# Kernel optimization log

Measured on AMD Instinct MI355X. Metric: run time of the kernel, lower is better.

Reference implementation:

```python
import jax, jax.numpy as jnp
import numpy as np

NFEAT = 128
NHID = 64
NLAYER = 3
N_NODES = 50000
N_EDGES = 800000
N_GRAPHS = 512
BN_EPS = 1e-5


def _bn(x, gamma, beta):
    # BatchNorm1d in training mode: biased batch stats over the node axis.
    m = x.mean(axis=0)
    v = x.var(axis=0)
    return (x - m) * jax.lax.rsqrt(v + BN_EPS) * gamma + beta


def _pool(x, batch):
    # global_mean_pool: segment mean over graph ids.
    s = jax.ops.segment_sum(x, batch, num_segments=N_GRAPHS)
    c = jax.ops.segment_sum(jnp.ones((x.shape[0], 1), x.dtype), batch, num_segments=N_GRAPHS)
    return s / jnp.maximum(c, 1.0)


def setup_inputs() -> dict:
    key = jax.random.key(0)
    ks = jax.random.split(key, 16)
    x = jax.random.normal(ks[0], (N_NODES, NFEAT), dtype=jnp.float32)
    edge_index = jax.random.randint(ks[1], (2, N_EDGES), 0, N_NODES, dtype=jnp.int64)
    batch = jnp.sort(jax.random.randint(ks[2], (N_NODES,), 0, N_GRAPHS, dtype=jnp.int64))
    s_in = 1.0 / np.sqrt(NFEAT)
    s_h = 1.0 / np.sqrt(NHID)
    return {
        "x": x,
        "edge_index": edge_index,
        "batch": batch,
        "Wt": jax.random.uniform(ks[3], (NFEAT, NHID), jnp.float32, -s_in, s_in),
        "bt": jax.random.uniform(ks[4], (NHID,), jnp.float32, -s_in, s_in),
        "gt": jnp.ones((NHID,), jnp.float32),
        "bet": jnp.zeros((NHID,), jnp.float32),
        "W1": jax.random.uniform(ks[5], (NLAYER, NHID, NHID), jnp.float32, -s_h, s_h),
        "b1": jax.random.uniform(ks[6], (NLAYER, NHID), jnp.float32, -s_h, s_h),
        "W2": jax.random.uniform(ks[7], (NLAYER, NHID, NHID), jnp.float32, -s_h, s_h),
        "b2": jax.random.uniform(ks[8], (NLAYER, NHID), jnp.float32, -s_h, s_h),
        "g": jnp.ones((NLAYER, NHID), jnp.float32),
        "be": jnp.zeros((NLAYER, NHID), jnp.float32),
    }


def reference(x, edge_index, batch, Wt, bt, gt, bet, W1, b1, W2, b2, g, be):
    n = x.shape[0]
    src, dst = edge_index[0], edge_index[1]
    # input transform: Linear + BN
    h = _bn(x @ Wt + bt, gt, bet)
    embeds = [_pool(h, batch)]
    for l in range(NLAYER):
        # GINConv, eps=0: mlp(x_i + sum_{j->i} x_j); flow source->target
        agg = jax.ops.segment_sum(h[src], dst, num_segments=n)
        z = h + agg
        z = jax.nn.relu(z @ W1[l] + b1[l]) @ W2[l] + b2[l]
        h = jax.nn.relu(_bn(z, g[l], be[l]))
        embeds.append(_pool(h, batch))
    return jnp.stack(embeds)  # [NLAYER+1, N_GRAPHS, NHID]
```

## Files before the change

### kernel.cpp

```cpp
#include <hip/hip_runtime.h>

#define NFEAT   128
#define NHID    64
#define NLAYER  3
#define NNODES  50000
#define NEDGES  800000
#define NGRAPHS 512
#define BN_EPS  1e-5f
#define MLPB    1563
#define CAP     64
#define PADW    68
#define FILLB   2048
#define SETUPB  83

typedef unsigned short u16;
typedef __attribute__((ext_vector_type(8))) short bf8;
typedef __attribute__((ext_vector_type(4))) float f32x4;

__device__ inline float b2f(u16 v) { return __uint_as_float(((unsigned)v) << 16); }
__device__ inline u16 f2b(float f) {
    unsigned u = __float_as_uint(f);
    return (u16)((u + 0x7FFF + ((u >> 16) & 1)) >> 16);
}
__device__ inline bf8 ldb8(const u16* p) {
    union { uint2 a[2]; bf8 v; } u;
    u.a[0] = *(const uint2*)p;
    u.a[1] = *(const uint2*)(p + 4);
    return u.v;
}
__device__ inline bf8 ldb8g(const u16* p) {
    union { uint4 a; bf8 v; } u;
    u.a = *(const uint4*)p;
    return u.v;
}
__device__ inline void add4(float* a, const uint2 v) {
    a[0] += __uint_as_float(v.x << 16);
    a[1] += __uint_as_float(v.x & 0xFFFF0000u);
    a[2] += __uint_as_float(v.y << 16);
    a[3] += __uint_as_float(v.y & 0xFFFF0000u);
}
__device__ inline void unp4(float* a, const uint2 v) {
    a[0] = __uint_as_float(v.x << 16);
    a[1] = __uint_as_float(v.x & 0xFFFF0000u);
    a[2] = __uint_as_float(v.y << 16);
    a[3] = __uint_as_float(v.y & 0xFFFF0000u);
}
__device__ inline void unp8(float* a, const uint4 v) {
    a[0] = __uint_as_float(v.x << 16);
    a[1] = __uint_as_float(v.x & 0xFFFF0000u);
    a[2] = __uint_as_float(v.y << 16);
    a[3] = __uint_as_float(v.y & 0xFFFF0000u);
    a[4] = __uint_as_float(v.z << 16);
    a[5] = __uint_as_float(v.z & 0xFFFF0000u);
    a[6] = __uint_as_float(v.w << 16);
    a[7] = __uint_as_float(v.w & 0xFFFF0000u);
}
__device__ inline uint2 pack4(float a, float b, float c, float d) {
    uint2 r;
    r.x = (unsigned)f2b(a) | ((unsigned)f2b(b) << 16);
    r.y = (unsigned)f2b(c) | ((unsigned)f2b(d) << 16);
    return r;
}

__global__ __launch_bounds__(256) void k_build(const int* __restrict__ ei,
                                               int* __restrict__ deg,
                                               u16* __restrict__ col,
                                               const float* __restrict__ Wt,
                                               const float* __restrict__ W1,
                                               const float* __restrict__ W2,
                                               const int* __restrict__ batch,
                                               u16* __restrict__ wtin,
                                               u16* __restrict__ wt,
                                               int* __restrict__ gstart) {
    int tid = threadIdx.x;
    if (blockIdx.x < FILLB) {
        int rangeId = blockIdx.x & 7, chunk = blockIdx.x >> 3;
        int lo = rangeId * (NNODES / 8), hi = lo + (NNODES / 8);
        int ebeg = chunk * (NEDGES / 256), eend = ebeg + (NEDGES / 256);
        int e = ebeg + tid;
        for (; e + 7 * 256 < eend; e += 8 * 256) {
            int d[8];
#pragma unroll
            for (int i = 0; i < 8; ++i) d[i] = ei[NEDGES + e + i * 256];
#pragma unroll
            for (int i = 0; i < 8; ++i) {
                if (d[i] >= lo && d[i] < hi) {
                    int s = atomicAdd(&deg[d[i]], 1);
                    if (s < CAP) col[d[i] * CAP + s] = (u16)ei[e + i * 256];
                }
            }
        }
        for (; e < eend; e += 256) {
            int dst = ei[NEDGES + e];
            if (dst >= lo && dst < hi) {
                int s = atomicAdd(&deg[dst], 1);
                if (s < CAP) col[dst * CAP + s] = (u16)ei[e];
            }
        }
        return;
    }
    int idx = (blockIdx.x - FILLB) * 256 + tid;
    if (idx < NFEAT * NHID) {
        int n = idx >> 7, k = idx & 127;
        wtin[n * NFEAT + k] = f2b(Wt[k * NHID + n]);
        return;
    }
    idx -= NFEAT * NHID;
    if (idx < NLAYER * NHID * NHID) {
        int l = idx >> 12, rem = idx & 4095, n = rem >> 6, k = rem & 63;
        wt[l * 8192 + n * 64 + k]        = f2b(W1[l * 4096 + k * 64 + n]);
        wt[l * 8192 + 4096 + n * 64 + k] = f2b(W2[l * 4096 + k * 64 + n]);
        return;
    }
    idx -= NLAYER * NHID * NHID;
    if (idx <= NGRAPHS) {
        if (idx == NGRAPHS) { gstart[NGRAPHS] = NNODES; return; }
        int lo = 0, hi = NNODES;
        while (lo < hi) {
            int mid = (lo + hi) >> 1;
            if (batch[mid] < idx) lo = mid + 1; else hi = mid;
        }
        gstart[idx] = lo;
    }
}

__global__ __launch_bounds__(256) void k_gemm_in(const float* __restrict__ x,
                                                 const u16* __restrict__ wtin,
                                                 const float* __restrict__ bt,
                                                 u16* __restrict__ zout,
                                                 float* __restrict__ partials) {
    __shared__ u16 sx[32][132];
    __shared__ float ps[128];
    int tid = threadIdx.x;
    int base = blockIdx.x * 32;
#pragma unroll
    for (int i = 0; i < 4; ++i) {
        int idx = i * 256 + tid;
        int row = idx >> 5, kq = idx & 31;
        int rc = min(base + row, NNODES - 1);
        float4 v = ((const float4*)(x + (long long)rc * NFEAT))[kq];
        *(uint2*)&sx[row][kq * 4] = pack4(v.x, v.y, v.z, v.w);
    }
    __syncthreads();
    int w = tid >> 6, lane = tid & 63;
    int m = lane & 15, g = lane >> 4;
    int ncol = w * 16 + m;
    bool hiv = (base + 16 < NNODES);
    float bb = bt[ncol];
    f32x4 cl = {bb, bb, bb, bb}, ch = {bb, bb, bb, bb};
    const u16* wn = wtin + ncol * NFEAT;
#pragma unroll
    for (int s = 0; s < 4; ++s) {
        int k0 = s * 32 + g * 8;
        bf8 B  = ldb8g(wn + k0);
        bf8 Al = ldb8(&sx[m][k0]);
        bf8 Ah = ldb8(&sx[16 + m][k0]);
        cl = __builtin_amdgcn_mfma_f32_16x16x32_bf16(Al, B, cl, 0, 0, 0);
        ch = __builtin_amdgcn_mfma_f32_16x16x32_bf16(Ah, B, ch, 0, 0, 0);
    }
    float s1 = cl[0] + cl[1] + cl[2] + cl[3];
    float s2 = cl[0] * cl[0] + cl[1] * cl[1] + cl[2] * cl[2] + cl[3] * cl[3];
    if (hiv) {
        s1 += ch[0] + ch[1] + ch[2] + ch[3];
        s2 += ch[0] * ch[0] + ch[1] * ch[1] + ch[2] * ch[2] + ch[3] * ch[3];
    }
    s1 += __shfl_xor(s1, 16, 64); s1 += __shfl_xor(s1, 32, 64);
    s2 += __shfl_xor(s2, 16, 64); s2 += __shfl_xor(s2, 32, 64);
    if (lane < 16) {
        ps[w * 16 + lane] = s1;
        ps[64 + w * 16 + lane] = s2;
    }
#pragma unroll
    for (int i = 0; i < 4; ++i) {
        zout[(base + g * 4 + i) * NHID + ncol] = f2b(cl[i]);
        if (hiv) zout[(base + 16 + g * 4 + i) * NHID + ncol] = f2b(ch[i]);
    }
    __syncthreads();
    if (tid < 128) partials[blockIdx.x * 128 + tid] = ps[tid];
}

__global__ __launch_bounds__(256) void k_red(const float* __restrict__ partials,
                                             float* __restrict__ stats, int np) {
    __shared__ float red[4];
    int c = blockIdx.x, t = threadIdx.x;
    float s = 0.f;
    for (int i = t; i < np; i += 256) s += partials[i * 128 + c];
#pragma unroll
    for (int off = 32; off >= 1; off >>= 1) s += __shfl_xor(s, off, 64);
    if ((t & 63) == 0) red[t >> 6] = s;
    __syncthreads();
    if (t == 0) stats[c] = red[0] + red[1] + red[2] + red[3];
}

__global__ __launch_bounds__(256) void k_bnh(const u16* __restrict__ z,
                                             const float* __restrict__ stats,
                                             const float* __restrict__ gamma,
                                             const float* __restrict__ beta,
                                             u16* __restrict__ h) {
    int idx = blockIdx.x * 256 + threadIdx.x;
    if (idx >= NNODES * NHID / 8) return;
    int j0 = (idx & 7) * 8;
    uint4 v = ((const uint4*)z)[idx];
    float o[8];
    unp8(o, v);
#pragma unroll
    for (int k = 0; k < 8; ++k) {
        int j = j0 + k;
        float m = stats[j] * (1.0f / NNODES);
        float var = stats[64 + j] * (1.0f / NNODES) - m * m;
        float sc = rsqrtf(var + BN_EPS) * gamma[j];
        o[k] = fmaxf(fmaf(o[k], sc, beta[j] - m * sc), 0.f);
    }
    uint4 w;
    uint2 p0 = pack4(o[0], o[1], o[2], o[3]);
    uint2 p1 = pack4(o[4], o[5], o[6], o[7]);
    w.x = p0.x; w.y = p0.y; w.z = p1.x; w.w = p1.y;
    ((uint4*)h)[idx] = w;
}

__global__ __launch_bounds__(256) void k_poolfin(const u16* __restrict__ z,
                                                 const float* __restrict__ stats,
                                                 const float* __restrict__ gamma,
                                                 const float* __restrict__ beta,
                                                 const int* __restrict__ gstart,
                                                 const float* __restrict__ poolacc,
                                                 float* __restrict__ out) {
    if (blockIdx.x >= NGRAPHS) {
        int idx = (int)(blockIdx.x - NGRAPHS) * 256 + threadIdx.x;
        if (idx < NLAYER * NGRAPHS * NHID) {
            int g = (idx >> 6) & (NGRAPHS - 1);
            float cnt = (float)(gstart[g + 1] - gstart[g]);
            out[idx] = poolacc[idx] / fmaxf(cnt, 1.0f);
        }
        return;
    }
    __shared__ float4 red[4][16];
    int gph = blockIdx.x;
    int lane = threadIdx.x & 63, w = threadIdx.x >> 6;
    int c = lane & 15, ws = lane >> 4;
    int slot = w * 4 + ws;
    int j0 = c * 4;
    float sc[4], sh[4];
#pragma unroll
    for (int k = 0; k < 4; ++k) {
        int j = j0 + k;
        float m = stats[j] * (1.0f / NNODES);
        float var = stats[64 + j] * (1.0f / NNODES) - m * m;
        sc[k] = rsqrtf(var + BN_EPS) * gamma[j];
        sh[k] = beta[j] - m * sc[k];
    }
    const ushort4* z4 = (const ushort4*)z;
    int s0 = gstart[gph], e0 = gstart[gph + 1];
    float a[4] = {0.f, 0.f, 0.f, 0.f};
    for (int r = s0 + slot; r < e0; r += 16) {
        ushort4 v = z4[r * 16 + c];
        a[0] += fmaxf(fmaf(b2f(v.x), sc[0], sh[0]), 0.f);
        a[1] += fmaxf(fmaf(b2f(v.y), sc[1], sh[1]), 0.f);
        a[2] += fmaxf(fmaf(b2f(v.z), sc[2], sh[2]), 0.f);
        a[3] += fmaxf(fmaf(b2f(v.w), sc[3], sh[3]), 0.f);
    }
#pragma unroll
    for (int k = 0; k < 4; ++k) {
        a[k] += __shfl_xor(a[k], 16, 64);
        a[k] += __shfl_xor(a[k], 32, 64);
    }
    if (lane < 16) red[w][c] = make_float4(a[0], a[1], a[2], a[3]);
    __syncthreads();
    if (threadIdx.x < 16) {
        float4 r0 = red[0][threadIdx.x], r1 = red[1][threadIdx.x];
        float4 r2 = red[2][threadIdx.x], r3 = red[3][threadIdx.x];
        float inv = 1.0f / fmaxf((float)(e0 - s0), 1.0f);
        float* o = &out[NLAYER * NGRAPHS * NHID + gph * NHID + threadIdx.x * 4];
        o[0] = (r0.x + r1.x + r2.x + r3.x) * inv;
        o[1] = (r0.y + r1.y + r2.y + r3.y) * inv;
        o[2] = (r0.z + r1.z + r2.z + r3.z) * inv;
        o[3] = (r0.w + r1.w + r2.w + r3.w) * inv;
    }
}

template <int AFFINE>
__global__ __launch_bounds__(512) void k_mlp(const u16* __restrict__ hin,
                                             const float* __restrict__ stats,
                                             const float* __restrict__ gamma,
                                             const float* __restrict__ beta,
                                             const int* __restrict__ batch,
                                             const int* __restrict__ deg,
                                             const u16* __restrict__ col,
                                             const u16* __restrict__ w1t,
                                             const float* __restrict__ b1,
                                             const u16* __restrict__ w2t,
                                             const float* __restrict__ b2,
                                             u16* __restrict__ zout,
                                             float* __restrict__ partials,
                                             float* __restrict__ poolacc) {
    __shared__ u16 szb[32][PADW];
    __shared__ u16 stb[32][PADW];
    __shared__ float ps2[2][128];
    int tid = threadIdx.x;
    int w = tid >> 6, lane = tid & 63;
    int nq = lane >> 4, c = lane & 15;
    int node = w * 4 + nq;
    int base = blockIdx.x * 32;
    int r = base + node;
    bool rv = (r < NNODES);
    int rc = rv ? r : (NNODES - 1);
    const uint2* h8 = (const uint2*)hin;

    float sc[4], sh[4];
    if (AFFINE) {
#pragma unroll
        for (int k = 0; k < 4; ++k) {
            int j = c * 4 + k;
            float m = stats[j] * (1.0f / NNODES);
            float var = stats[64 + j] * (1.0f / NNODES) - m * m;
            sc[k] = rsqrtf(var + BN_EPS) * gamma[j];
            sh[k] = beta[j] - m * sc[k];
        }
    }

    float acc[4], acc2[4] = {0, 0, 0, 0};
    float selfh[4];
    {
        uint2 sv = h8[rc * 16 + c];
        unp4(acc, sv);
#pragma unroll
        for (int k = 0; k < 4; ++k)
            selfh[k] = AFFINE ? fmaf(acc[k], sc[k], sh[k]) : acc[k];
    }
    int dd = rv ? min(deg[r], CAP) : 0;
    {
        const u16* cp = col + rc * CAP;
        int t = 0;
        for (; t + 8 <= dd; t += 8) {
            uint4 iv = *(const uint4*)(cp + t);
            int s0 = iv.x & 0xFFFF, s1 = iv.x >> 16;
            int s2 = iv.y & 0xFFFF, s3 = iv.y >> 16;
            int s4 = iv.z & 0xFFFF, s5 = iv.z >> 16;
            int s6 = iv.w & 0xFFFF, s7 = iv.w >> 16;
            uint2 v0 = h8[s0 * 16 + c];
            uint2 v1 = h8[s1 * 16 + c];
            uint2 v2 = h8[s2 * 16 + c];
            uint2 v3 = h8[s3 * 16 + c];
            uint2 v4 = h8[s4 * 16 + c];
            uint2 v5 = h8[s5 * 16 + c];
            uint2 v6 = h8[s6 * 16 + c];
            uint2 v7 = h8[s7 * 16 + c];
            add4(acc, v0); add4(acc2, v1); add4(acc, v2); add4(acc2, v3);
            add4(acc, v4); add4(acc2, v5); add4(acc, v6); add4(acc2, v7);
        }
        if (t + 4 <= dd) {
            uint2 iv = *(const uint2*)(cp + t);
            int s0 = iv.x & 0xFFFF, s1 = iv.x >> 16;
            int s2 = iv.y & 0xFFFF, s3 = iv.y >> 16;
            uint2 v0 = h8[s0 * 16 + c];
            uint2 v1 = h8[s1 * 16 + c];
            uint2 v2 = h8[s2 * 16 + c];
            uint2 v3 = h8[s3 * 16 + c];
            add4(acc, v0); add4(acc2, v1); add4(acc, v2); add4(acc2, v3);
            t += 4;
        }
        for (; t < dd; ++t) {
            uint2 v0 = h8[(int)cp[t] * 16 + c];
            add4(acc, v0);
        }
    }
    {
        float zv[4];
#pragma unroll
        for (int k = 0; k < 4; ++k) {
            float s = acc[k] + acc2[k];
            zv[k] = AFFINE ? fmaf(s, sc[k], (float)(1 + dd) * sh[k]) : s;
            if (!rv) zv[k] = 0.f;
        }
        *(uint2*)&szb[node][c * 4] = pack4(zv[0], zv[1], zv[2], zv[3]);
    }

    int m = lane & 15, g = lane >> 4;
    int half = w >> 2, cg = w & 3;
    int ncol = cg * 16 + m;
    const u16* w1n = w1t + ncol * 64;
    const u16* w2n = w2t + ncol * 64;
    bf8 B0 = ldb8g(w1n + g * 8);
    bf8 B1 = ldb8g(w1n + 32 + g * 8);
    bf8 D0 = ldb8g(w2n + g * 8);
    bf8 D1 = ldb8g(w2n + 32 + g * 8);

    {
        int r0 = base + w * 4;
        int myg = rv ? batch[r] : -1;
        int g_lo = batch[min(r0, NNODES - 1)];
        int g_hi = batch[min(r0 + 3, NNODES - 1)];
        for (int gg = g_lo; gg <= g_hi; ++gg) {
            float v[4];
#pragma unroll
            for (int k = 0; k < 4; ++k) {
                v[k] = (myg == gg) ? selfh[k] : 0.f;
                v[k] += __shfl_xor(v[k], 16, 64);
                v[k] += __shfl_xor(v[k], 32, 64);
            }
            if (lane < 16) {
                float* p = &poolacc[gg * NHID + lane * 4];
#pragma unroll
                for (int k = 0; k < 4; ++k) atomicAdd(p + k, v[k]);
            }
        }
    }
    __syncthreads();

    bool hiv = (base + 16 < NNODES);
    bool halfv = (half == 0) || hiv;
    bf8 A0 = ldb8(&szb[half * 16 + m][g * 8]);
    bf8 A1 = ldb8(&szb[half * 16 + m][32 + g * 8]);
    float bb1 = b1[ncol];
    f32x4 c1 = {bb1, bb1, bb1, bb1};
    c1 = __builtin_amdgcn_mfma_f32_16x16x32_bf16(A0, B0, c1, 0, 0, 0);
    c1 = __builtin_amdgcn_mfma_f32_16x16x32_bf16(A1, B1, c1, 0, 0, 0);
#pragma unroll
    for (int i = 0; i < 4; ++i)
        stb[half * 16 + g * 4 + i][ncol] = f2b(fmaxf(c1[i], 0.f));
    __syncthreads();

    bf8 C0 = ldb8(&stb[half * 16 + m][g * 8]);
    bf8 C1 = ldb8(&stb[half * 16 + m][32 + g * 8]);
    float bb2 = b2[ncol];
    f32x4 e = {bb2, bb2, bb2, bb2};
    e = __builtin_amdgcn_mfma_f32_16x16x32_bf16(C0, D0, e, 0, 0, 0);
    e = __builtin_amdgcn_mfma_f32_16x16x32_bf16(C1, D1, e, 0, 0, 0);

    float s1 = e[0] + e[1] + e[2] + e[3];
    float s2 = e[0] * e[0] + e[1] * e[1] + e[2] * e[2] + e[3] * e[3];
    if (!halfv) { s1 = 0.f; s2 = 0.f; }
    s1 += __shfl_xor(s1, 16, 64); s1 += __shfl_xor(s1, 32, 64);
    s2 += __shfl_xor(s2, 16, 64); s2 += __shfl_xor(s2, 32, 64);
    if (lane < 16) {
        ps2[half][cg * 16 + lane] = s1;
        ps2[half][64 + cg * 16 + lane] = s2;
    }
    if (halfv) {
#pragma unroll
        for (int i = 0; i < 4; ++i)
            zout[(base + half * 16 + g * 4 + i) * NHID + ncol] = f2b(e[i]);
    }
    __syncthreads();
    if (tid < 128) partials[blockIdx.x * 128 + tid] = ps2[0][tid] + ps2[1][tid];
}

extern "C" void kernel_launch(void* const* d_in, const int* in_sizes, int n_in,
                              void* d_out, int out_size, void* d_ws, size_t ws_size,
                              hipStream_t stream) {
    const float* x     = (const float*)d_in[0];
    const int*   ei    = (const int*)d_in[1];
    const int*   batch = (const int*)d_in[2];
    const float* Wt    = (const float*)d_in[3];
    const float* bt    = (const float*)d_in[4];
    const float* gt    = (const float*)d_in[5];
    const float* bet   = (const float*)d_in[6];
    const float* W1    = (const float*)d_in[7];
    const float* b1    = (const float*)d_in[8];
    const float* W2    = (const float*)d_in[9];
    const float* b2    = (const float*)d_in[10];
    const float* g     = (const float*)d_in[11];
    const float* be    = (const float*)d_in[12];
    float* out = (float*)d_out;

    u16* A          = (u16*)d_ws;
    u16* B          = A + NNODES * NHID;
    u16* H          = B + NNODES * NHID;
    u16* wt         = H + NNODES * NHID;
    u16* wtin       = wt + NLAYER * 2 * NHID * NHID;
    float* partials = (float*)(wtin + NFEAT * NHID);
    float* stats    = partials + MLPB * 128;
    int* deg        = (int*)(stats + 4 * 128);
    float* poolacc  = (float*)(deg + NNODES);
    u16* col        = (u16*)(poolacc + NLAYER * NGRAPHS * NHID);
    int* gstart     = (int*)(col + NNODES * CAP);

    size_t zbytes = NNODES * sizeof(int) + NLAYER * NGRAPHS * NHID * sizeof(float);
    hipMemsetAsync(deg, 0, zbytes, stream);

    k_build<<<FILLB + SETUPB, 256, 0, stream>>>(ei, deg, col, Wt, W1, W2, batch,
                                                wtin, wt, gstart);

    k_gemm_in<<<MLPB, 256, 0, stream>>>(x, wtin, bt, A, partials);
    k_red<<<128, 256, 0, stream>>>(partials, stats, MLPB);

    k_mlp<1><<<MLPB, 512, 0, stream>>>(A, stats, gt, bet, batch, deg, col,
                                       wt, b1, wt + 4096, b2,
                                       B, partials, poolacc);
    k_red<<<128, 256, 0, stream>>>(partials, stats + 128, MLPB);

    k_bnh<<<MLPB, 256, 0, stream>>>(B, stats + 128, g, be, H);
    k_mlp<0><<<MLPB, 512, 0, stream>>>(H, stats + 128, g, be, batch, deg, col,
                                       wt + 8192, b1 + NHID, wt + 8192 + 4096, b2 + NHID,
                                       A, partials, poolacc + NGRAPHS * NHID);
    k_red<<<128, 256, 0, stream>>>(partials, stats + 256, MLPB);

    k_bnh<<<MLPB, 256, 0, stream>>>(A, stats + 256, g + NHID, be + NHID, H);
    k_mlp<0><<<MLPB, 512, 0, stream>>>(H, stats + 256, g + NHID, be + NHID, batch, deg, col,
                                       wt + 16384, b1 + 2 * NHID, wt + 16384 + 4096, b2 + 2 * NHID,
                                       B, partials, poolacc + 2 * NGRAPHS * NHID);
    k_red<<<128, 256, 0, stream>>>(partials, stats + 384, MLPB);

    k_poolfin<<<NGRAPHS + (NLAYER * NGRAPHS * NHID + 255) / 256, 256, 0, stream>>>(
        B, stats + 384, g + 2 * NHID, be + 2 * NHID, gstart, poolacc, out);
}
```

Baseline: 189.3 us.

## Fuse input GEMM into graph-build kernel, converting Wt to bf16 on the fly

Merges the input linear layer kernel into the edge-bucketing/setup kernel as extra blocks, so one launch covers CSR fill, weight conversion and the input GEMM. To break the dependency on the pre-transposed bf16 Wt, each GEMM block now reads fp32 Wt directly with strided loads and converts it in registers. This removes one kernel launch and its inter-kernel gap and lets the GEMM overlap with the atomic-heavy fill. The cost is uncoalesced, redundant Wt reads in every GEMM block, plus shared memory now allocated for all blocks, including fill blocks.

```diff
diff --git a/kernel.cpp b/kernel.cpp
--- a/kernel.cpp
+++ b/kernel.cpp
@@ -11,7 +11,7 @@
 #define CAP     64
 #define PADW    68
 #define FILLB   2048
-#define SETUPB  83
+#define SETUPB  51
 
 typedef unsigned short u16;
 typedef __attribute__((ext_vector_type(8))) short bf8;
@@ -62,16 +62,21 @@
     return r;
 }
 
-__global__ __launch_bounds__(256) void k_build(const int* __restrict__ ei,
-                                               int* __restrict__ deg,
-                                               u16* __restrict__ col,
-                                               const float* __restrict__ Wt,
-                                               const float* __restrict__ W1,
-                                               const float* __restrict__ W2,
-                                               const int* __restrict__ batch,
-                                               u16* __restrict__ wtin,
-                                               u16* __restrict__ wt,
-                                               int* __restrict__ gstart) {
+__global__ __launch_bounds__(256) void k_buildgemm(const int* __restrict__ ei,
+                                                   int* __restrict__ deg,
+                                                   u16* __restrict__ col,
+                                                   const float* __restrict__ Wt,
+                                                   const float* __restrict__ W1,
+                                                   const float* __restrict__ W2,
+                                                   const int* __restrict__ batch,
+                                                   u16* __restrict__ wt,
+                                                   int* __restrict__ gstart,
+                                                   const float* __restrict__ x,
+                                                   const float* __restrict__ bt,
+                                                   u16* __restrict__ zout,
+                                                   float* __restrict__ partials) {
+    __shared__ u16 sx[32][132];
+    __shared__ float ps[128];
     int tid = threadIdx.x;
     if (blockIdx.x < FILLB) {
         int rangeId = blockIdx.x & 7, chunk = blockIdx.x >> 3;
@@ -99,40 +104,28 @@
         }
         return;
     }
-    int idx = (blockIdx.x - FILLB) * 256 + tid;
-    if (idx < NFEAT * NHID) {
-        int n = idx >> 7, k = idx & 127;
-        wtin[n * NFEAT + k] = f2b(Wt[k * NHID + n]);
+    if (blockIdx.x < FILLB + SETUPB) {
+        int idx = (blockIdx.x - FILLB) * 256 + tid;
+        if (idx < NLAYER * NHID * NHID) {
+            int l = idx >> 12, rem = idx & 4095, n = rem >> 6, k = rem & 63;
+            wt[l * 8192 + n * 64 + k]        = f2b(W1[l * 4096 + k * 64 + n]);
+            wt[l * 8192 + 4096 + n * 64 + k] = f2b(W2[l * 4096 + k * 64 + n]);
+            return;
+        }
+        idx -= NLAYER * NHID * NHID;
+        if (idx <= NGRAPHS) {
+            if (idx == NGRAPHS) { gstart[NGRAPHS] = NNODES; return; }
+            int lo = 0, hi = NNODES;
+            while (lo < hi) {
+                int mid = (lo + hi) >> 1;
+                if (batch[mid] < idx) lo = mid + 1; else hi = mid;
+            }
+            gstart[idx] = lo;
+        }
         return;
     }
-    idx -= NFEAT * NHID;
-    if (idx < NLAYER * NHID * NHID) {
-        int l = idx >> 12, rem = idx & 4095, n = rem >> 6, k = rem & 63;
-        wt[l * 8192 + n * 64 + k]        = f2b(W1[l * 4096 + k * 64 + n]);
-        wt[l * 8192 + 4096 + n * 64 + k] = f2b(W2[l * 4096 + k * 64 + n]);
-        return;
-    }
-    idx -= NLAYER * NHID * NHID;
-    if (idx <= NGRAPHS) {
-        if (idx == NGRAPHS) { gstart[NGRAPHS] = NNODES; return; }
-        int lo = 0, hi = NNODES;
-        while (lo < hi) {
-            int mid = (lo + hi) >> 1;
-            if (batch[mid] < idx) lo = mid + 1; else hi = mid;
-        }
-        gstart[idx] = lo;
-    }
-}
-
-__global__ __launch_bounds__(256) void k_gemm_in(const float* __restrict__ x,
-                                                 const u16* __restrict__ wtin,
-                                                 const float* __restrict__ bt,
-                                                 u16* __restrict__ zout,
-                                                 float* __restrict__ partials) {
-    __shared__ u16 sx[32][132];
-    __shared__ float ps[128];
-    int tid = threadIdx.x;
-    int base = blockIdx.x * 32;
+    int vb = blockIdx.x - FILLB - SETUPB;
+    int base = vb * 32;
 #pragma unroll
     for (int i = 0; i < 4; ++i) {
         int idx = i * 256 + tid;
@@ -148,11 +141,14 @@
     bool hiv = (base + 16 < NNODES);
     float bb = bt[ncol];
     f32x4 cl = {bb, bb, bb, bb}, ch = {bb, bb, bb, bb};
-    const u16* wn = wtin + ncol * NFEAT;
-#pragma unroll
-    for (int s = 0; s < 4; ++s) {
-        int k0 = s * 32 + g * 8;
-        bf8 B  = ldb8g(wn + k0);
+    const float* wnf = Wt + ncol;
+#pragma unroll
+    for (int s4 = 0; s4 < 4; ++s4) {
+        int k0 = s4 * 32 + g * 8;
+        union { u16 t[8]; bf8 v; } ub;
+#pragma unroll
+        for (int i = 0; i < 8; ++i) ub.t[i] = f2b(wnf[(k0 + i) * NHID]);
+        bf8 B = ub.v;
         bf8 Al = ldb8(&sx[m][k0]);
         bf8 Ah = ldb8(&sx[16 + m][k0]);
         cl = __builtin_amdgcn_mfma_f32_16x16x32_bf16(Al, B, cl, 0, 0, 0);
@@ -176,7 +172,7 @@
         if (hiv) zout[(base + 16 + g * 4 + i) * NHID + ncol] = f2b(ch[i]);
     }
     __syncthreads();
-    if (tid < 128) partials[blockIdx.x * 128 + tid] = ps[tid];
+    if (tid < 128) partials[vb * 128 + tid] = ps[tid];
 }
 
 __global__ __launch_bounds__(256) void k_red(const float* __restrict__ partials,
@@ -467,8 +463,7 @@
     u16* B          = A + NNODES * NHID;
     u16* H          = B + NNODES * NHID;
     u16* wt         = H + NNODES * NHID;
-    u16* wtin       = wt + NLAYER * 2 * NHID * NHID;
-    float* partials = (float*)(wtin + NFEAT * NHID);
+    float* partials = (float*)(wt + NLAYER * 2 * NHID * NHID);
     float* stats    = partials + MLPB * 128;
     int* deg        = (int*)(stats + 4 * 128);
     float* poolacc  = (float*)(deg + NNODES);
@@ -478,10 +473,8 @@
     size_t zbytes = NNODES * sizeof(int) + NLAYER * NGRAPHS * NHID * sizeof(float);
     hipMemsetAsync(deg, 0, zbytes, stream);
 
-    k_build<<<FILLB + SETUPB, 256, 0, stream>>>(ei, deg, col, Wt, W1, W2, batch,
-                                                wtin, wt, gstart);
-
-    k_gemm_in<<<MLPB, 256, 0, stream>>>(x, wtin, bt, A, partials);
+    k_buildgemm<<<FILLB + SETUPB + MLPB, 256, 0, stream>>>(
+        ei, deg, col, Wt, W1, W2, batch, wt, gstart, x, bt, A, partials);
     k_red<<<128, 256, 0, stream>>>(partials, stats, MLPB);
 
     k_mlp<1><<<MLPB, 512, 0, stream>>>(A, stats, gt, bet, batch, deg, col,
```

New measurement: 182.8 us, median of 2. 3.4% less time.
